# Kernel tuning notes

Hardware: AMD Instinct MI355X
Metric: run time of the kernel (lower is better)

The kernel has to match this reference:

```python
import jax, jax.numpy as jnp
import numpy as np

NUM_GRAPHS = 512

def gcn_conv(x, src, dst, W, b, n):
    # x: [N, Fin], W: [Fin, Fout]. PyG GCNConv: add self loops, symmetric norm.
    h = x @ W  # [N, Fout]
    loop = jnp.arange(n)
    s = jnp.concatenate([src, loop])
    d = jnp.concatenate([dst, loop])
    ones = jnp.ones(s.shape[0], dtype=h.dtype)
    deg = jax.ops.segment_sum(ones, d, num_segments=n)  # includes self loop -> >= 1
    dinv = jax.lax.rsqrt(deg)
    norm = dinv[s] * dinv[d]  # [E+N]
    msg = h[s] * norm[:, None]  # gather + scale (memory-bound)
    out = jax.ops.segment_sum(msg, d, num_segments=n)
    return out + b

def setup_inputs() -> dict:
    key = jax.random.key(0)
    ks = jax.random.split(key, 10)
    N, E, F, H, O, EF = 100000, 1600000, 128, 128, 1, 16
    x = jax.random.normal(ks[0], (N, F), dtype=jnp.float32)
    edge_index = jax.random.randint(ks[1], (2, E), 0, N)
    edge_attr = jax.random.normal(ks[2], (E, EF), dtype=jnp.float32)
    batch = jnp.sort(jax.random.randint(ks[3], (N,), 0, NUM_GRAPHS))
    s1 = 1.0 / np.sqrt(F)
    s2 = 1.0 / np.sqrt(H)
    W1 = jax.random.uniform(ks[4], (F, H), jnp.float32, -s1, s1)
    b1 = jnp.zeros((H,), jnp.float32)
    W2 = jax.random.uniform(ks[5], (H, H), jnp.float32, -s2, s2)
    b2 = jnp.zeros((H,), jnp.float32)
    Wl = jax.random.uniform(ks[6], (H, O), jnp.float32, -s2, s2)
    bl = jnp.zeros((O,), jnp.float32)
    return {"x": x, "edge_index": edge_index, "edge_attr": edge_attr, "batch": batch,
            "W1": W1, "b1": b1, "W2": W2, "b2": b2, "Wl": Wl, "bl": bl}

def reference(x, edge_index, edge_attr, batch, W1, b1, W2, b2, Wl, bl):
    n = x.shape[0]
    src, dst = edge_index[0], edge_index[1]
    h = jax.nn.relu(gcn_conv(x, src, dst, W1, b1, n))
    h = gcn_conv(h, src, dst, W2, b2, n)
    # global mean pool by graph id
    summed = jax.ops.segment_sum(h, batch, num_segments=NUM_GRAPHS)  # [G, H]
    counts = jax.ops.segment_sum(jnp.ones((n,), h.dtype), batch, num_segments=NUM_GRAPHS)
    pooled = summed / jnp.maximum(counts, 1.0)[:, None]
    return pooled @ Wl + bl  # [G, 1]
```

## Files before the change

kernel.cpp:

```cpp
#include <hip/hip_runtime.h>


typedef __attribute__((ext_vector_type(8))) short short8;
typedef __attribute__((ext_vector_type(4))) float f32x4;

#define CHUNK 4096
#define RW    128
#define SCAP  6144
#define JCAP  512

__device__ __forceinline__ unsigned short bf16r(float f) {
    unsigned u = __float_as_uint(f);
    u += 0x7FFFu + ((u >> 16) & 1u);
    return (unsigned short)(u >> 16);
}

__device__ __forceinline__ float bff(unsigned short u) {
    return __uint_as_float((unsigned)u << 16);
}

__global__ void k_w1pack(const float* __restrict__ W1, unsigned short* __restrict__ w1p,
                         const float* __restrict__ W2, const float* __restrict__ Wl,
                         float* __restrict__ w2l) {
    if (blockIdx.x == 64) {
        int i = threadIdx.x;
        if (i < 128) {
            float s = 0.0f;
            for (int j = 0; j < 128; ++j) s = fmaf(W2[i * 128 + j], Wl[j], s);
            w2l[i] = s;
        }
        return;
    }
    int idx = blockIdx.x * 256 + threadIdx.x;
    int k = idx >> 7, n = idx & 127;
    w1p[((k >> 3) * 128 + n) * 8 + (k & 7)] = bf16r(W1[idx]);
}

__global__ __launch_bounds__(256) void k_part(
    const int* __restrict__ src, const int* __restrict__ dst,
    int* __restrict__ part, int* __restrict__ off_t, int* __restrict__ cnt_t,
    int E, int nchunks, int NR)
{
    __shared__ int stage[CHUNK];
    __shared__ int lcnt[1024];
    __shared__ int lscan[1024];
    int tid = threadIdx.x;
    int j = blockIdx.x;
    int base = j * CHUNK;

#pragma unroll
    for (int k = 0; k < 4; ++k) lcnt[tid + k * 256] = 0;
    __syncthreads();

    int mye[16], myr[16];
#pragma unroll
    for (int k = 0; k < 16; ++k) {
        int e = base + tid + (k << 8);
        bool ok = e < E;
        int s = ok ? src[e] : 0;
        int d = ok ? dst[e] : 0;
        int r = -1;
        if (ok) {
            r = d >> 7;
            atomicAdd(&lcnt[r], 1);
        }
        mye[k] = (s << 7) | (d & 127);
        myr[k] = r;
    }
    __syncthreads();

    int* pa = lcnt;
    int* pb = lscan;
    for (int off = 1; off < 1024; off <<= 1) {
#pragma unroll
        for (int k = 0; k < 4; ++k) {
            int idx = tid + k * 256;
            int v = pa[idx];
            if (idx >= off) v += pa[idx - off];
            pb[idx] = v;
        }
        __syncthreads();
        int* tmp = pa; pa = pb; pb = tmp;
    }
    for (int i = tid; i < NR; i += 256) {
        int incl = pa[i];
        int excl = (i == 0) ? 0 : pa[i - 1];
        pb[i] = excl;
        off_t[(size_t)i * nchunks + j] = excl;
        cnt_t[(size_t)i * nchunks + j] = incl - excl;
    }
    __syncthreads();

#pragma unroll
    for (int k = 0; k < 16; ++k) {
        if (myr[k] >= 0) {
            int p = atomicAdd(&pb[myr[k]], 1);
            stage[p] = mye[k];
        }
    }
    __syncthreads();

    int valid = E - base; if (valid > CHUNK) valid = CHUNK;
    for (int i = tid; i < valid; i += 256)
        part[(size_t)base + i] = stage[i];
}

__global__ __launch_bounds__(64) void k_rtot(
    const int* __restrict__ cnt_t, int* __restrict__ rtot, int nchunks)
{
    int r = blockIdx.x;
    int lane = threadIdx.x;
    const int* row = cnt_t + (size_t)r * nchunks;
    int s = 0;
    for (int j = lane; j < nchunks; j += 64) s += row[j];
#pragma unroll
    for (int off = 32; off > 0; off >>= 1) s += __shfl_xor(s, off);
    if (lane == 0) rtot[r] = s;
}

__global__ __launch_bounds__(1024) void k_rbase(
    const int* __restrict__ rtot, int* __restrict__ rbase, int NR)
{
    __shared__ int a1[1024], a2[1024];
    int tid = threadIdx.x;
    a1[tid] = (tid < NR) ? rtot[tid] : 0;
    __syncthreads();
    int* pa = a1; int* pb = a2;
    for (int off = 1; off < 1024; off <<= 1) {
        int v = pa[tid];
        if (tid >= off) v += pa[tid - off];
        pb[tid] = v;
        __syncthreads();
        int* tmp = pa; pa = pb; pb = tmp;
    }
    if (tid < NR) rbase[tid] = (tid == 0) ? 0 : pa[tid - 1];
    if (tid == 0) rbase[NR] = pa[NR >= 1 ? NR - 1 : 0];
}

__global__ __launch_bounds__(256) void k_rscat(
    const int* __restrict__ part, const int* __restrict__ off_t,
    const int* __restrict__ cnt_t, const int* __restrict__ rbase,
    int* __restrict__ srt, int* __restrict__ rp, float* __restrict__ dinv,
    int nchunks, int N, int E)
{
    __shared__ int stage[SCAP];
    __shared__ int jbase[JCAP];
    __shared__ int hist[RW], lcur[RW], s1[RW], s2[RW];
    __shared__ int cursor;
    int r = blockIdx.x;
    int tid = threadIdx.x;
    int d0 = r << 7;
    int width = N - d0; if (width > RW) width = RW;
    if (tid < RW) hist[tid] = 0;
    if (tid == 0) cursor = 0;
    __syncthreads();

    const int* orow = off_t + (size_t)r * nchunks;
    const int* crow = cnt_t + (size_t)r * nchunks;

    for (int j = tid; j < nchunks; j += 256) {
        int c = crow[j];
        if (c == 0) { if (j < JCAP) jbase[j] = 0; continue; }
        int b = (j < JCAP) ? atomicAdd(&cursor, c) : SCAP;
        if (j < JCAP) jbase[j] = b;
        const int* pp = part + (size_t)j * CHUNK + orow[j];
        for (int e = 0; e < c; ++e) {
            int ed = pp[e];
            int pos = b + e;
            if (pos < SCAP) stage[pos] = ed;
            atomicAdd(&hist[ed & 127], 1);
        }
    }
    __syncthreads();
    int total = cursor;

    if (tid < RW) s1[tid] = hist[tid];
    __syncthreads();
    int* pa = s1; int* pb = s2;
    for (int off = 1; off < RW; off <<= 1) {
        if (tid < RW) {
            int v = pa[tid];
            if (tid >= off) v += pa[tid - off];
            pb[tid] = v;
        }
        __syncthreads();
        int* tmp = pa; pa = pb; pb = tmp;
    }
    if (tid < width) {
        int excl = (tid == 0) ? 0 : pa[tid - 1];
        int start = rbase[r] + excl;
        rp[d0 + tid] = start;
        lcur[tid] = start;
        dinv[d0 + tid] = 1.0f / sqrtf((float)hist[tid] + 1.0f);
    }
    if (r == 0 && tid == 0) rp[N] = E;
    __syncthreads();

    int lim = total < SCAP ? total : SCAP;
    for (int i = tid; i < lim; i += 256) {
        int ed = stage[i];
        int pos = atomicAdd(&lcur[ed & 127], 1);
        srt[pos] = ed >> 7;
    }
    if (total > SCAP || nchunks > JCAP) {
        for (int j = tid; j < nchunks; j += 256) {
            int c = crow[j];
            if (c == 0) continue;
            int e0 = 0;
            if (j < JCAP) {
                int b = jbase[j];
                e0 = SCAP - b;
                if (e0 < 0) e0 = 0;
                if (e0 >= c) continue;
            }
            const int* pp = part + (size_t)j * CHUNK + orow[j];
            for (int e = e0; e < c; ++e) {
                int ed = pp[e];
                int pos = atomicAdd(&lcur[ed & 127], 1);
                srt[pos] = ed >> 7;
            }
        }
    }
}

__global__ __launch_bounds__(256) void k_mm_mfma(
    const float* __restrict__ A, const unsigned short* __restrict__ w1p,
    const float* __restrict__ dinv, unsigned short* __restrict__ C, int N)
{
    __shared__ unsigned short w1s[16384];
    int tid = threadIdx.x;
    {
        const uint4* s = (const uint4*)w1p;
        uint4* d = (uint4*)w1s;
#pragma unroll
        for (int i = 0; i < 8; ++i) d[tid + i * 256] = s[tid + i * 256];
    }
    __syncthreads();

    int w = tid >> 6, lane = tid & 63;
    int m = lane & 15, quad = lane >> 4;
    int r0 = blockIdx.x * 128 + w * 32;

    f32x4 acc[2][8];
#pragma unroll
    for (int rg = 0; rg < 2; ++rg)
#pragma unroll
        for (int cg = 0; cg < 8; ++cg) {
            f32x4 z = {0.0f, 0.0f, 0.0f, 0.0f};
            acc[rg][cg] = z;
        }

#pragma unroll
    for (int ks = 0; ks < 4; ++ks) {
        int k0 = ks * 32 + quad * 8;
        short8 a[2];
#pragma unroll
        for (int rg = 0; rg < 2; ++rg) {
            int r = r0 + rg * 16 + m;
            if (r > N - 1) r = N - 1;
            const float* ap = A + (size_t)r * 128 + k0;
            float4 v0 = *(const float4*)ap;
            float4 v1 = *(const float4*)(ap + 4);
            short8 av;
            av[0] = (short)bf16r(v0.x); av[1] = (short)bf16r(v0.y);
            av[2] = (short)bf16r(v0.z); av[3] = (short)bf16r(v0.w);
            av[4] = (short)bf16r(v1.x); av[5] = (short)bf16r(v1.y);
            av[6] = (short)bf16r(v1.z); av[7] = (short)bf16r(v1.w);
            a[rg] = av;
        }
        int kc = ks * 4 + quad;
#pragma unroll
        for (int cg = 0; cg < 8; ++cg) {
            const short8* bp = (const short8*)&w1s[((size_t)kc * 128 + cg * 16 + m) * 8];
            short8 b = *bp;
            acc[0][cg] = __builtin_amdgcn_mfma_f32_16x16x32_bf16(a[0], b, acc[0][cg], 0, 0, 0);
            acc[1][cg] = __builtin_amdgcn_mfma_f32_16x16x32_bf16(a[1], b, acc[1][cg], 0, 0, 0);
        }
    }

#pragma unroll
    for (int rg = 0; rg < 2; ++rg) {
        int rbase2 = r0 + rg * 16 + quad * 4;
#pragma unroll
        for (int reg = 0; reg < 4; ++reg) {
            int r = rbase2 + reg;
            if (r < N) {
                float s = dinv[r];
#pragma unroll
                for (int cg = 0; cg < 8; ++cg)
                    C[(size_t)r * 128 + cg * 16 + m] = bf16r(acc[rg][cg][reg] * s);
            }
        }
    }
}

__global__ __launch_bounds__(256) void k_agg1(
    const unsigned short* __restrict__ t, const float* __restrict__ dinv,
    const int* __restrict__ rp, const int* __restrict__ srt,
    const float* __restrict__ b1, const float* __restrict__ w2l,
    float* __restrict__ q, int N, int nwaves)
{
    __shared__ int shi[4][2][64];
    int wave = threadIdx.x >> 6;
    int lane = threadIdx.x & 63;
    int gw = blockIdx.x * 4 + wave;
    if (gw >= N) return;

    int r4 = lane >> 4;
    int c = lane & 15;
    const unsigned short* tc = t + c * 8;

    float4 b0 = *(const float4*)(b1 + c * 8);
    float4 b4 = *(const float4*)(b1 + c * 8 + 4);
    float4 w0 = *(const float4*)(w2l + c * 8);
    float4 w4 = *(const float4*)(w2l + c * 8 + 4);

    int node = gw;
    int s0 = rp[node], s1 = rp[node + 1];
    float di = dinv[node];
    {
        int deg = s1 - s0;
        int vdeg = deg < 63 ? deg : 63;
        int idx = N;
        if (lane < vdeg) idx = srt[s0 + lane];
        else if (lane == vdeg) idx = node;
        shi[wave][0][lane] = idx;
    }
    int buf = 0;

    while (true) {
        int nnode = node + nwaves;
        int ns0 = 0, ns1 = 0, nidx = N;
        float ndi = 0.0f;
        bool have_next = nnode < N;
        if (have_next) {
            ns0 = rp[nnode]; ns1 = rp[nnode + 1];
            ndi = dinv[nnode];
            int ndeg = ns1 - ns0;
            int nvdeg = ndeg < 63 ? ndeg : 63;
            if (lane < nvdeg) nidx = srt[ns0 + lane];
            else if (lane == nvdeg) nidx = nnode;
        }

        const int* shw = shi[wave][buf];
        int deg = s1 - s0;
        int vdeg = deg < 63 ? deg : 63;
        float a[8];
#pragma unroll
        for (int k = 0; k < 8; ++k) a[k] = 0.0f;
        int nrows = vdeg + 1;
        int nquads = (nrows + 3) >> 2;
        int p = 0;
        do {
            short8 v[8];
#pragma unroll
            for (int j = 0; j < 8; ++j) {
                int id = shw[((p + j) << 2) + r4];
                v[j] = *(const short8*)(tc + (size_t)id * 128);
            }
#pragma unroll
            for (int j = 0; j < 8; ++j)
#pragma unroll
                for (int k = 0; k < 8; ++k)
                    a[k] += bff((unsigned short)v[j][k]);
            p += 8;
        } while (p < nquads);

        if (deg > 63) {
            for (int e = s0 + 63; e < s1; ++e) {
                int id = srt[e];
                short8 v = *(const short8*)(tc + (size_t)id * 128);
                if (r4 == 0)
#pragma unroll
                    for (int k = 0; k < 8; ++k)
                        a[k] += bff((unsigned short)v[k]);
            }
        }

#pragma unroll
        for (int k = 0; k < 8; ++k) {
            a[k] += __shfl_xor(a[k], 16);
            a[k] += __shfl_xor(a[k], 32);
        }

        float pr = 0.0f;
        pr += fmaxf(fmaf(a[0], di, b0.x), 0.0f) * w0.x;
        pr += fmaxf(fmaf(a[1], di, b0.y), 0.0f) * w0.y;
        pr += fmaxf(fmaf(a[2], di, b0.z), 0.0f) * w0.z;
        pr += fmaxf(fmaf(a[3], di, b0.w), 0.0f) * w0.w;
        pr += fmaxf(fmaf(a[4], di, b4.x), 0.0f) * w4.x;
        pr += fmaxf(fmaf(a[5], di, b4.y), 0.0f) * w4.y;
        pr += fmaxf(fmaf(a[6], di, b4.z), 0.0f) * w4.z;
        pr += fmaxf(fmaf(a[7], di, b4.w), 0.0f) * w4.w;
#pragma unroll
        for (int off = 8; off > 0; off >>= 1) pr += __shfl_xor(pr, off);
        if (lane == 0) q[node] = pr * di;

        if (!have_next) break;
        shi[wave][buf ^ 1][lane] = nidx;
        node = nnode; s0 = ns0; s1 = ns1; di = ndi; buf ^= 1;
    }
}

__global__ __launch_bounds__(256) void k_agg2(
    const float* __restrict__ q, const float* __restrict__ dinv,
    const int* __restrict__ rp, const int* __restrict__ srt,
    float* __restrict__ p, int N)
{
    int tid = blockIdx.x * 256 + threadIdx.x;
    int node = tid >> 4;
    int l = tid & 15;
    if (node >= N) return;
    int s0 = rp[node], s1 = rp[node + 1];
    float a = 0.0f;
    for (int e = s0 + l; e < s1; e += 16) a += q[srt[e]];
#pragma unroll
    for (int off = 8; off > 0; off >>= 1) a += __shfl_xor(a, off);
    if (l == 0) p[node] = dinv[node] * (a + q[node]);
}

__global__ __launch_bounds__(64) void k_pool(
    const float* __restrict__ p, const int* __restrict__ batch,
    const float* __restrict__ b2, const float* __restrict__ Wl,
    const float* __restrict__ bl, float* __restrict__ out, int N, int G)
{
    int g = blockIdx.x;
    int lane = threadIdx.x;
    __shared__ int sb[2];
    if (lane < 2) {
        int target = g + lane;
        int lo = 0, hi = N;
        while (lo < hi) {
            int mid = (lo + hi) >> 1;
            if (batch[mid] < target) lo = mid + 1; else hi = mid;
        }
        sb[lane] = lo;
    }
    __syncthreads();
    int s = sb[0], e = sb[1];
    float a = 0.0f;
    for (int i = s + lane; i < e; i += 64) a += p[i];
#pragma unroll
    for (int off = 32; off > 0; off >>= 1) a += __shfl_xor(a, off);
    if (lane == 0) {
        float c = 0.0f;
        for (int j = 0; j < 128; ++j) c = fmaf(b2[j], Wl[j], c);
        out[g] = a / fmaxf((float)(e - s), 1.0f) + c + bl[0];
    }
}

extern "C" void kernel_launch(void* const* d_in, const int* in_sizes, int n_in,
                              void* d_out, int out_size, void* d_ws, size_t ws_size,
                              hipStream_t stream)
{
    const float* x  = (const float*)d_in[0];
    const int*   ei = (const int*)d_in[1];
    const int*   batch = (const int*)d_in[3];
    const float* W1 = (const float*)d_in[4];
    const float* b1 = (const float*)d_in[5];
    const float* W2 = (const float*)d_in[6];
    const float* b2 = (const float*)d_in[7];
    const float* Wl = (const float*)d_in[8];
    const float* bl = (const float*)d_in[9];

    int N = in_sizes[0] / 128;
    int E = in_sizes[1] / 2;
    const int* src = ei;
    const int* dst = ei + E;

    char* ws = (char*)d_ws;
    size_t off = 0;
    auto alloc = [&](size_t bytes) -> void* {
        void* p = ws + off;
        off = (off + bytes + 255) & ~(size_t)255;
        return p;
    };
    int nchunks = (E + CHUNK - 1) / CHUNK;
    int NR = (N + RW - 1) / RW;
    unsigned short* t = (unsigned short*)alloc((size_t)(N + 1) * 128 * 2);
    float* q    = (float*)alloc((size_t)N * 4);
    float* p    = (float*)alloc((size_t)N * 4);
    int*   srt  = (int*)alloc((size_t)E * 4);
    int*   part = (int*)alloc((size_t)nchunks * CHUNK * 4);
    int*   off_t= (int*)alloc((size_t)NR * nchunks * 4);
    int*   cnt_t= (int*)alloc((size_t)NR * nchunks * 4);
    int*   rtot = (int*)alloc((size_t)NR * 4);
    int*   rbase= (int*)alloc((size_t)(NR + 1) * 4);
    float* dinv = (float*)alloc((size_t)N * 4);
    int*   rp   = (int*)alloc((size_t)(N + 1) * 4);
    float* w2l  = (float*)alloc(128 * 4);
    unsigned short* w1p = (unsigned short*)alloc(16384 * 2);
    (void)ws_size;

    hipMemsetAsync(t + (size_t)N * 128, 0, 256, stream);

    k_part<<<nchunks, 256, 0, stream>>>(src, dst, part, off_t, cnt_t, E, nchunks, NR);
    k_w1pack<<<65, 256, 0, stream>>>(W1, w1p, W2, Wl, w2l);
    k_rtot<<<NR, 64, 0, stream>>>(cnt_t, rtot, nchunks);
    k_rbase<<<1, 1024, 0, stream>>>(rtot, rbase, NR);
    k_rscat<<<NR, 256, 0, stream>>>(part, off_t, cnt_t, rbase, srt, rp, dinv,
                                    nchunks, N, E);

    int mmb = (N + 127) / 128;
    k_mm_mfma<<<mmb, 256, 0, stream>>>(x, w1p, dinv, t, N);
    int a1b = 2048;
    k_agg1<<<a1b, 256, 0, stream>>>(t, dinv, rp, srt, b1, w2l, q, N, a1b * 4);
    k_agg2<<<((size_t)N * 16 + 255) / 256, 256, 0, stream>>>(q, dinv, rp, srt, p, N);
    k_pool<<<512, 64, 0, stream>>>(p, batch, b2, Wl, bl, (float*)d_out, N, 512);
}
```

Before: 336.1 us.

## Fuse CSR build with feature matmul and drop global row-offset scan

Folds the W1 packing and W2·Wl precompute into the edge partition kernel as extra blocks. The per-row-block totals and prefix-scan kernels are removed: each 128-node row block now writes its edges into a fixed-capacity slot (WCAP), and per-node start and end arrays replace the single row-pointer array. The bf16 MFMA matmul moves into the CSR build kernel, using the block's own dinv values from shared memory, and the sentinel row is zeroed in-kernel instead of by a memset. This removes several launches and global round-trips, at the cost of much larger shared memory per block (lower occupancy). Any row block with more than 6144 incoming edges would silently overflow into its neighbour's slot.

```diff
diff --git a/kernel.cpp b/kernel.cpp
--- a/kernel.cpp
+++ b/kernel.cpp
@@ -8,6 +8,7 @@
 #define RW    128
 #define SCAP  6144
 #define JCAP  512
+#define WCAP  6144
 
 __device__ __forceinline__ unsigned short bf16r(float f) {
     unsigned u = __float_as_uint(f);
@@ -19,32 +20,33 @@
     return __uint_as_float((unsigned)u << 16);
 }
 
-__global__ void k_w1pack(const float* __restrict__ W1, unsigned short* __restrict__ w1p,
-                         const float* __restrict__ W2, const float* __restrict__ Wl,
-                         float* __restrict__ w2l) {
-    if (blockIdx.x == 64) {
-        int i = threadIdx.x;
-        if (i < 128) {
-            float s = 0.0f;
-            for (int j = 0; j < 128; ++j) s = fmaf(W2[i * 128 + j], Wl[j], s);
-            w2l[i] = s;
-        }
-        return;
-    }
-    int idx = blockIdx.x * 256 + threadIdx.x;
-    int k = idx >> 7, n = idx & 127;
-    w1p[((k >> 3) * 128 + n) * 8 + (k & 7)] = bf16r(W1[idx]);
-}
-
-__global__ __launch_bounds__(256) void k_part(
+__global__ __launch_bounds__(256) void k_partw(
     const int* __restrict__ src, const int* __restrict__ dst,
     int* __restrict__ part, int* __restrict__ off_t, int* __restrict__ cnt_t,
-    int E, int nchunks, int NR)
-{
+    const float* __restrict__ W1, unsigned short* __restrict__ w1p,
+    const float* __restrict__ W2, const float* __restrict__ Wl,
+    float* __restrict__ w2l, int E, int nchunks, int NR)
+{
+    int tid = threadIdx.x;
+    if (blockIdx.x >= nchunks) {
+        int b = blockIdx.x - nchunks;
+        if (b == 64) {
+            if (tid < 128) {
+                float s = 0.0f;
+                for (int j = 0; j < 128; ++j) s = fmaf(W2[tid * 128 + j], Wl[j], s);
+                w2l[tid] = s;
+            }
+            return;
+        }
+        int idx = b * 256 + tid;
+        int k = idx >> 7, n = idx & 127;
+        w1p[((k >> 3) * 128 + n) * 8 + (k & 7)] = bf16r(W1[idx]);
+        return;
+    }
+
     __shared__ int stage[CHUNK];
     __shared__ int lcnt[1024];
     __shared__ int lscan[1024];
-    int tid = threadIdx.x;
     int j = blockIdx.x;
     int base = j * CHUNK;
 
@@ -105,52 +107,30 @@
         part[(size_t)base + i] = stage[i];
 }
 
-__global__ __launch_bounds__(64) void k_rtot(
-    const int* __restrict__ cnt_t, int* __restrict__ rtot, int nchunks)
-{
-    int r = blockIdx.x;
-    int lane = threadIdx.x;
-    const int* row = cnt_t + (size_t)r * nchunks;
-    int s = 0;
-    for (int j = lane; j < nchunks; j += 64) s += row[j];
-#pragma unroll
-    for (int off = 32; off > 0; off >>= 1) s += __shfl_xor(s, off);
-    if (lane == 0) rtot[r] = s;
-}
-
-__global__ __launch_bounds__(1024) void k_rbase(
-    const int* __restrict__ rtot, int* __restrict__ rbase, int NR)
-{
-    __shared__ int a1[1024], a2[1024];
-    int tid = threadIdx.x;
-    a1[tid] = (tid < NR) ? rtot[tid] : 0;
-    __syncthreads();
-    int* pa = a1; int* pb = a2;
-    for (int off = 1; off < 1024; off <<= 1) {
-        int v = pa[tid];
-        if (tid >= off) v += pa[tid - off];
-        pb[tid] = v;
-        __syncthreads();
-        int* tmp = pa; pa = pb; pb = tmp;
-    }
-    if (tid < NR) rbase[tid] = (tid == 0) ? 0 : pa[tid - 1];
-    if (tid == 0) rbase[NR] = pa[NR >= 1 ? NR - 1 : 0];
-}
-
-__global__ __launch_bounds__(256) void k_rscat(
+__global__ __launch_bounds__(256) void k_build(
     const int* __restrict__ part, const int* __restrict__ off_t,
-    const int* __restrict__ cnt_t, const int* __restrict__ rbase,
-    int* __restrict__ srt, int* __restrict__ rp, float* __restrict__ dinv,
-    int nchunks, int N, int E)
+    const int* __restrict__ cnt_t, const float* __restrict__ x,
+    const unsigned short* __restrict__ w1p, int* __restrict__ srt,
+    int* __restrict__ rps, int* __restrict__ rpe, float* __restrict__ dinv,
+    unsigned short* __restrict__ t, int nchunks, int N, int NR)
 {
     __shared__ int stage[SCAP];
     __shared__ int jbase[JCAP];
     __shared__ int hist[RW], lcur[RW], s1[RW], s2[RW];
+    __shared__ float dins[RW];
     __shared__ int cursor;
+    __shared__ unsigned short w1s[16384];
     int r = blockIdx.x;
     int tid = threadIdx.x;
     int d0 = r << 7;
     int width = N - d0; if (width > RW) width = RW;
+
+    {
+        const uint4* s = (const uint4*)w1p;
+        uint4* d = (uint4*)w1s;
+#pragma unroll
+        for (int i = 0; i < 8; ++i) d[tid + i * 256] = s[tid + i * 256];
+    }
     if (tid < RW) hist[tid] = 0;
     if (tid == 0) cursor = 0;
     __syncthreads();
@@ -186,14 +166,18 @@
         __syncthreads();
         int* tmp = pa; pa = pb; pb = tmp;
     }
+    int wbase = r * WCAP;
     if (tid < width) {
         int excl = (tid == 0) ? 0 : pa[tid - 1];
-        int start = rbase[r] + excl;
-        rp[d0 + tid] = start;
+        int start = wbase + excl;
+        int deg = hist[tid];
+        rps[d0 + tid] = start;
+        rpe[d0 + tid] = start + deg;
         lcur[tid] = start;
-        dinv[d0 + tid] = 1.0f / sqrtf((float)hist[tid] + 1.0f);
-    }
-    if (r == 0 && tid == 0) rp[N] = E;
+        float di = 1.0f / sqrtf((float)deg + 1.0f);
+        dins[tid] = di;
+        dinv[d0 + tid] = di;
+    }
     __syncthreads();
 
     int lim = total < SCAP ? total : SCAP;
@@ -221,25 +205,10 @@
             }
         }
     }
-}
-
-__global__ __launch_bounds__(256) void k_mm_mfma(
-    const float* __restrict__ A, const unsigned short* __restrict__ w1p,
-    const float* __restrict__ dinv, unsigned short* __restrict__ C, int N)
-{
-    __shared__ unsigned short w1s[16384];
-    int tid = threadIdx.x;
-    {
-        const uint4* s = (const uint4*)w1p;
-        uint4* d = (uint4*)w1s;
-#pragma unroll
-        for (int i = 0; i < 8; ++i) d[tid + i * 256] = s[tid + i * 256];
-    }
-    __syncthreads();
 
     int w = tid >> 6, lane = tid & 63;
     int m = lane & 15, quad = lane >> 4;
-    int r0 = blockIdx.x * 128 + w * 32;
+    int r0 = d0 + w * 32;
 
     f32x4 acc[2][8];
 #pragma unroll
@@ -256,9 +225,9 @@
         short8 a[2];
 #pragma unroll
         for (int rg = 0; rg < 2; ++rg) {
-            int r = r0 + rg * 16 + m;
-            if (r > N - 1) r = N - 1;
-            const float* ap = A + (size_t)r * 128 + k0;
+            int rr = r0 + rg * 16 + m;
+            if (rr > N - 1) rr = N - 1;
+            const float* ap = x + (size_t)rr * 128 + k0;
             float4 v0 = *(const float4*)ap;
             float4 v1 = *(const float4*)(ap + 4);
             short8 av;
@@ -280,23 +249,29 @@
 
 #pragma unroll
     for (int rg = 0; rg < 2; ++rg) {
-        int rbase2 = r0 + rg * 16 + quad * 4;
+        int rb = r0 + rg * 16 + quad * 4;
 #pragma unroll
         for (int reg = 0; reg < 4; ++reg) {
-            int r = rbase2 + reg;
-            if (r < N) {
-                float s = dinv[r];
+            int row = rb + reg;
+            if (row < N) {
+                float s = dins[row - d0];
 #pragma unroll
                 for (int cg = 0; cg < 8; ++cg)
-                    C[(size_t)r * 128 + cg * 16 + m] = bf16r(acc[rg][cg][reg] * s);
-            }
-        }
+                    t[(size_t)row * 128 + cg * 16 + m] = bf16r(acc[rg][cg][reg] * s);
+            }
+        }
+    }
+
+    if (r == NR - 1 && tid < 16) {
+        uint4 z = {0u, 0u, 0u, 0u};
+        ((uint4*)(t + (size_t)N * 128))[tid] = z;
     }
 }
 
 __global__ __launch_bounds__(256) void k_agg1(
     const unsigned short* __restrict__ t, const float* __restrict__ dinv,
-    const int* __restrict__ rp, const int* __restrict__ srt,
+    const int* __restrict__ rps, const int* __restrict__ rpe,
+    const int* __restrict__ srt,
     const float* __restrict__ b1, const float* __restrict__ w2l,
     float* __restrict__ q, int N, int nwaves)
 {
@@ -316,7 +291,7 @@
     float4 w4 = *(const float4*)(w2l + c * 8 + 4);
 
     int node = gw;
-    int s0 = rp[node], s1 = rp[node + 1];
+    int s0 = rps[node], s1 = rpe[node];
     float di = dinv[node];
     {
         int deg = s1 - s0;
@@ -334,7 +309,7 @@
         float ndi = 0.0f;
         bool have_next = nnode < N;
         if (have_next) {
-            ns0 = rp[nnode]; ns1 = rp[nnode + 1];
+            ns0 = rps[nnode]; ns1 = rpe[nnode];
             ndi = dinv[nnode];
             int ndeg = ns1 - ns0;
             int nvdeg = ndeg < 63 ? ndeg : 63;
@@ -404,14 +379,14 @@
 
 __global__ __launch_bounds__(256) void k_agg2(
     const float* __restrict__ q, const float* __restrict__ dinv,
-    const int* __restrict__ rp, const int* __restrict__ srt,
-    float* __restrict__ p, int N)
+    const int* __restrict__ rps, const int* __restrict__ rpe,
+    const int* __restrict__ srt, float* __restrict__ p, int N)
 {
     int tid = blockIdx.x * 256 + threadIdx.x;
     int node = tid >> 4;
     int l = tid & 15;
     if (node >= N) return;
-    int s0 = rp[node], s1 = rp[node + 1];
+    int s0 = rps[node], s1 = rpe[node];
     float a = 0.0f;
     for (int e = s0 + l; e < s1; e += 16) a += q[srt[e]];
 #pragma unroll
@@ -480,31 +455,23 @@
     unsigned short* t = (unsigned short*)alloc((size_t)(N + 1) * 128 * 2);
     float* q    = (float*)alloc((size_t)N * 4);
     float* p    = (float*)alloc((size_t)N * 4);
-    int*   srt  = (int*)alloc((size_t)E * 4);
+    int*   srt  = (int*)alloc((size_t)NR * WCAP * 4);
     int*   part = (int*)alloc((size_t)nchunks * CHUNK * 4);
     int*   off_t= (int*)alloc((size_t)NR * nchunks * 4);
     int*   cnt_t= (int*)alloc((size_t)NR * nchunks * 4);
-    int*   rtot = (int*)alloc((size_t)NR * 4);
-    int*   rbase= (int*)alloc((size_t)(NR + 1) * 4);
     float* dinv = (float*)alloc((size_t)N * 4);
-    int*   rp   = (int*)alloc((size_t)(N + 1) * 4);
+    int*   rps  = (int*)alloc((size_t)N * 4);
+    int*   rpe  = (int*)alloc((size_t)N * 4);
     float* w2l  = (float*)alloc(128 * 4);
     unsigned short* w1p = (unsigned short*)alloc(16384 * 2);
     (void)ws_size;
 
-    hipMemsetAsync(t + (size_t)N * 128, 0, 256, stream);
-
-    k_part<<<nchunks, 256, 0, stream>>>(src, dst, part, off_t, cnt_t, E, nchunks, NR);
-    k_w1pack<<<65, 256, 0, stream>>>(W1, w1p, W2, Wl, w2l);
-    k_rtot<<<NR, 64, 0, stream>>>(cnt_t, rtot, nchunks);
-    k_rbase<<<1, 1024, 0, stream>>>(rtot, rbase, NR);
-    k_rscat<<<NR, 256, 0, stream>>>(part, off_t, cnt_t, rbase, srt, rp, dinv,
-                                    nchunks, N, E);
-
-    int mmb = (N + 127) / 128;
-    k_mm_mfma<<<mmb, 256, 0, stream>>>(x, w1p, dinv, t, N);
+    k_partw<<<nchunks + 65, 256, 0, stream>>>(src, dst, part, off_t, cnt_t,
+                                              W1, w1p, W2, Wl, w2l, E, nchunks, NR);
+    k_build<<<NR, 256, 0, stream>>>(part, off_t, cnt_t, x, w1p, srt, rps, rpe,
+                                    dinv, t, nchunks, N, NR);
     int a1b = 2048;
-    k_agg1<<<a1b, 256, 0, stream>>>(t, dinv, rp, srt, b1, w2l, q, N, a1b * 4);
-    k_agg2<<<((size_t)N * 16 + 255) / 256, 256, 0, stream>>>(q, dinv, rp, srt, p, N);
+    k_agg1<<<a1b, 256, 0, stream>>>(t, dinv, rps, rpe, srt, b1, w2l, q, N, a1b * 4);
+    k_agg2<<<((size_t)N * 16 + 255) / 256, 256, 0, stream>>>(q, dinv, rps, rpe, srt, p, N);
     k_pool<<<512, 64, 0, stream>>>(p, batch, b2, Wl, bl, (float*)d_out, N, 512);
 }
```

Result: no change. 332.6 us (-1.0%).
